# Optimization experiments

Hardware: AMD Instinct MI355X
Metric: run time of the kernel (lower is better)

## Reference

```python
import math
import jax, jax.numpy as jnp
import numpy as np

B, C, K, P, STRIDE, ITERS = 32, 32, 3, 4, 2, 3
PSIZE = P * P
EPS = 1e-6
LAMBDA = 1e-3
LN_2PI = math.log(2.0 * math.pi)


def _extract_patches(x, K, stride):
    # Replicates torch F.unfold + transpose + view exactly, including the
    # layout reinterpretation: unfold's channel dim is ordered (c, kh, kw)
    # (c slowest) but the torch code views it as (K*K, c).
    b, h, w, c = x.shape
    pad = K // 2
    oh = (h + 2 * pad - K) // stride + 1
    ow = (w + 2 * pad - K) // stride + 1
    xp = jnp.pad(x, ((0, 0), (pad, pad), (pad, pad), (0, 0)))
    sl = []
    for kh in range(K):
        for kw in range(K):
            sl.append(xp[:, kh:kh + stride * (oh - 1) + 1:stride,
                            kw:kw + stride * (ow - 1) + 1:stride, :])
    p = jnp.stack(sl, axis=-1)                 # (b, oh, ow, c, K*K)  -> (c, kh, kw) order
    p = p.reshape(b, oh, ow, c * K * K)        # flat, c slowest (matches torch unfold memory)
    patches = p.reshape(b, oh, ow, K * K, c)   # reinterpret as (K*K, c), as the torch view does
    return patches, oh, ow


def _em_routing(v, a_in, beta_u, beta_a):
    # v: (b, Bin, C, psize), a_in: (b, Bin, 1)
    b, Bin, Cc, psize = v.shape
    r = jnp.full((b, Bin, Cc, 1), 1.0 / Cc, dtype=v.dtype)
    a4 = a_in[:, :, None, :]                   # (b, Bin, 1, 1)
    a_out = None
    mu = None
    for t in range(ITERS):
        # ---- M step ----
        rr = r * a4
        rr = rr / (jnp.sum(rr, axis=2, keepdims=True) + EPS)
        r_sum = jnp.sum(rr, axis=1, keepdims=True)            # (b,1,C,1)
        coeff = rr / (r_sum + EPS)
        mu = jnp.sum(coeff * v, axis=1, keepdims=True)        # (b,1,C,psize)
        sigma_sq = jnp.sum(coeff * (v - mu) ** 2, axis=1, keepdims=True) + EPS
        sigma_sq = jnp.maximum(sigma_sq, 1e-4)
        r_sum_flat = r_sum.reshape(b, Cc, 1)
        sig_flat = jnp.maximum(sigma_sq.reshape(b, Cc, psize), 1e-4)
        cost_h = (beta_u.reshape(1, Cc, 1) + jnp.log(jnp.sqrt(sig_flat))) * r_sum_flat
        a_out = jax.nn.sigmoid(LAMBDA * (beta_a.reshape(1, Cc) - jnp.sum(cost_h, axis=2)))
        a_out = jnp.clip(a_out, 1e-4, 1.0 - 1e-4)
        mu = jnp.nan_to_num(mu, nan=0.0, posinf=1e4, neginf=-1e4)
        sigma_sq = jnp.nan_to_num(sigma_sq, nan=1e-4, posinf=1e4, neginf=1e-4)
        a_out = jnp.nan_to_num(a_out, nan=0.5, posinf=1.0 - 1e-4, neginf=1e-4)
        # ---- E step ----
        if t < ITERS - 1:
            ss = jnp.maximum(sigma_sq, 1e-4)
            ao = jnp.clip(a_out, 1e-4, 1.0 - 1e-4)
            ln_p = -(v - mu) ** 2 / (2.0 * ss) - jnp.log(jnp.sqrt(ss)) - 0.5 * LN_2PI
            ln_ap = jnp.sum(ln_p, axis=3) + jnp.log(ao.reshape(b, 1, Cc) + EPS)
            ln_ap = jnp.nan_to_num(ln_ap, nan=0.0, posinf=50.0, neginf=-50.0)
            r = jax.nn.softmax(ln_ap, axis=2)[..., None]
            r = jnp.nan_to_num(r, nan=1.0 / Cc, posinf=1.0, neginf=0.0)
    p_out = jnp.nan_to_num(mu[:, 0], nan=0.0, posinf=1e4, neginf=-1e4)  # (b, C, psize)
    a_out = jnp.nan_to_num(a_out, nan=0.5, posinf=1.0 - 1e-4, neginf=1e-4)
    return p_out, a_out


def setup_inputs() -> dict:
    key = jax.random.key(0)
    k1, k2 = jax.random.split(key)
    x = jax.random.normal(k1, (2, 16, 16, B * (PSIZE + 1)), dtype=jnp.float32)
    weights = jax.random.normal(k2, (1, K * K * B, C, PSIZE, PSIZE), dtype=jnp.float32) * 0.02
    beta_u = jnp.zeros((C,), dtype=jnp.float32)
    beta_a = jnp.zeros((C,), dtype=jnp.float32)
    return {"x": x, "weights": weights, "beta_u": beta_u, "beta_a": beta_a}


def reference(x, weights, beta_u, beta_a):
    b, h, w, c = x.shape
    patches, oh, ow = _extract_patches(x, K, STRIDE)          # (b,oh,ow,K*K,c)
    p_in = patches[..., :B * PSIZE].reshape(b * oh * ow, K * K * B, PSIZE)
    a_in = patches[..., B * PSIZE:].reshape(b * oh * ow, K * K * B, 1)
    w0 = weights[0]                                           # (K*K*B, C, psize, psize)
    v = jnp.einsum('bip,icpq->bicq', p_in, w0)                # (b*, K*K*B, C, psize)
    p_out, a_out = _em_routing(v, a_in, beta_u, beta_a)
    p_out = p_out.reshape(b, oh, ow, C * PSIZE)
    a_out = a_out.reshape(b, oh, ow, C)
    out = jnp.concatenate([p_out, a_out], axis=3)
    return p_out, a_out, out
```

## Files before the change

kernel.cpp:

```cpp
#include <hip/hip_runtime.h>
#include <hip/hip_bf16.h>
#include <math.h>

#define EPSV 1e-6f
#define LAMBDAV 1e-3f
#define LN_2PI 1.8378770664093453f

__device__ __forceinline__ float bflo(unsigned int u) {
    union { unsigned int i; float f; } x; x.i = u << 16; return x.f;
}
__device__ __forceinline__ float bfhi(unsigned int u) {
    union { unsigned int i; float f; } x; x.i = u & 0xffff0000u; return x.f;
}
__device__ __forceinline__ unsigned short f2bf(float f) {
    __hip_bfloat16 h = __float2bfloat16(f);
    return *(unsigned short*)&h;
}

typedef __attribute__((ext_vector_type(8))) short s8v;
typedef __attribute__((ext_vector_type(4))) float f4v;
typedef __attribute__((ext_vector_type(2))) int i2v;

template<int CTRL>
__device__ __forceinline__ float dpp_mv(float x) {
    return __int_as_float(__builtin_amdgcn_update_dpp(
        0, __float_as_int(x), CTRL, 0xF, 0xF, true));
}
__device__ __forceinline__ float x16_sum(float x) {
#if __has_builtin(__builtin_amdgcn_permlane16_swap)
    i2v r = __builtin_amdgcn_permlane16_swap(__float_as_int(x), __float_as_int(x), false, false);
    return __int_as_float(r.x) + __int_as_float(r.y);
#else
    return x + __int_as_float(__builtin_amdgcn_ds_swizzle(__float_as_int(x), 0x401F));
#endif
}
__device__ __forceinline__ float x16_max(float x) {
#if __has_builtin(__builtin_amdgcn_permlane16_swap)
    i2v r = __builtin_amdgcn_permlane16_swap(__float_as_int(x), __float_as_int(x), false, false);
    return fmaxf(__int_as_float(r.x), __int_as_float(r.y));
#else
    return fmaxf(x, __int_as_float(__builtin_amdgcn_ds_swizzle(__float_as_int(x), 0x401F)));
#endif
}
__device__ __forceinline__ float xhalf_sum(float x) {
#if __has_builtin(__builtin_amdgcn_permlane32_swap)
    i2v r = __builtin_amdgcn_permlane32_swap(__float_as_int(x), __float_as_int(x), false, false);
    return __int_as_float(r.x) + __int_as_float(r.y);
#else
    return x + __shfl_xor(x, 32, 64);
#endif
}
__device__ __forceinline__ float red_max32(float x) {
    x = fmaxf(x, dpp_mv<0xB1>(x));
    x = fmaxf(x, dpp_mv<0x4E>(x));
    x = fmaxf(x, dpp_mv<0x124>(x));
    x = fmaxf(x, dpp_mv<0x128>(x));
    return x16_max(x);
}
__device__ __forceinline__ float red_sum32(float x) {
    x += dpp_mv<0xB1>(x);
    x += dpp_mv<0x4E>(x);
    x += dpp_mv<0x124>(x);
    x += dpp_mv<0x128>(x);
    return x16_sum(x);
}
__device__ __forceinline__ float red_sum16(float x) {
    x += dpp_mv<0xB1>(x);
    x += dpp_mv<0x4E>(x);
    x += dpp_mv<0x124>(x);
    x += dpp_mv<0x128>(x);
    return x;
}

__global__ __launch_bounds__(256)
void conv_v_kernel(const float* __restrict__ x, const float* __restrict__ w,
                   __hip_bfloat16* __restrict__ vout)
{
    __shared__ unsigned short wb[256 * 40];
    __shared__ unsigned short pb[128 * 40];
    __shared__ unsigned short st[16 * 264];

    const int bid = blockIdx.x;
    const int i2  = bid >> 1;
    const int mh  = bid & 1;
    const int tid = threadIdx.x;

    for (int u = tid; u < 256 * 8; u += 256) {
        int r = u >> 3, j = u & 7;
        *(unsigned int*)&wb[r * 40 + 16 + j * 2] = 0;
    }
    for (int u = tid; u < 128 * 8; u += 256) {
        int r = u >> 3, j = u & 7;
        *(unsigned int*)&pb[r * 40 + 16 + j * 2] = 0;
    }
    #pragma unroll 4
    for (int u = 0; u < 16; ++u) {
        int idx = u * 256 + tid;
        int cl = idx >> 8, p = (idx >> 4) & 15, q = idx & 15;
        wb[(cl * 16 + q) * 40 + p] = f2bf(w[(size_t)i2 * 8192 + mh * 4096 + idx]);
    }
    #pragma unroll
    for (int u = 0; u < 8; ++u) {
        int idx = u * 256 + tid;
        int nn = idx >> 4, p = idx & 15;
        int e  = i2 * 16 + p;
        int k2 = e >> 9, c2 = e & 511;
        int f  = k2 * 544 + c2;
        int ci = f / 9, kk = f - ci * 9;
        int bi = nn >> 6, oi = (nn >> 3) & 7, oj = nn & 7;
        int row = 2 * oi + kk / 3 - 1;
        int col = 2 * oj + (kk - (kk / 3) * 3) - 1;
        float val = 0.f;
        if ((unsigned)row < 16u && (unsigned)col < 16u)
            val = x[((bi * 16 + row) * 16 + col) * 544 + ci];
        pb[nn * 40 + p] = f2bf(val);
    }
    __syncthreads();

    const int lane = tid & 63;
    const int wv   = tid >> 6;
    const int l16  = lane & 15;
    const int quad = lane >> 4;
    const int cq0l = wv * 64;

    s8v afrag[4], bfrag[8];
    #pragma unroll
    for (int mt = 0; mt < 4; ++mt)
        afrag[mt] = *(const s8v*)&wb[(cq0l + mt * 16 + l16) * 40 + quad * 8];
    #pragma unroll
    for (int nt = 0; nt < 8; ++nt)
        bfrag[nt] = *(const s8v*)&pb[(nt * 16 + l16) * 40 + quad * 8];

    const int srow = tid >> 4;
    const int schk = tid & 15;
    #pragma unroll
    for (int nt = 0; nt < 8; ++nt) {
        #pragma unroll
        for (int mt = 0; mt < 4; ++mt) {
            f4v acc = {0.f, 0.f, 0.f, 0.f};
            acc = __builtin_amdgcn_mfma_f32_16x16x32_bf16(afrag[mt], bfrag[nt], acc, 0, 0, 0);
            int ccol = cq0l + mt * 16 + quad * 4;
            unsigned int lo = f2bf(acc[0]) | ((unsigned int)f2bf(acc[1]) << 16);
            unsigned int hi = f2bf(acc[2]) | ((unsigned int)f2bf(acc[3]) << 16);
            uint2 pk; pk.x = lo; pk.y = hi;
            *(uint2*)&st[l16 * 264 + ccol] = pk;
        }
        __syncthreads();
        {
            uint4 d0 = *(const uint4*)&st[srow * 264 + schk * 16];
            uint4 d1 = *(const uint4*)&st[srow * 264 + schk * 16 + 8];
            int nl = nt * 16 + srow;
            unsigned short* dst = (unsigned short*)vout
                + ((size_t)nl * 288 + i2) * 512 + mh * 256 + schk * 16;
            *(uint4*)dst = d0;
            *(uint4*)(dst + 8) = d1;
        }
        __syncthreads();
    }
}

__global__ __launch_bounds__(512)
void em_sweep_kernel(const float* __restrict__ x,
                     const unsigned short* __restrict__ v,
                     const float* __restrict__ beta_u,
                     const float* __restrict__ beta_a,
                     float* __restrict__ gpart,
                     const int t)
{
    __shared__ float fct_s[288];
    __shared__ float red_s[8 * 64 * 17];
    __shared__ float mu_s[32 * 17];
    __shared__ float i2ss_s[32 * 17];
    __shared__ float kc_s[32];

    const int bid = blockIdx.x;
    const int n   = bid & 127;
    const int h   = bid >> 7;
    const int tid = threadIdx.x;
    const int bi = n >> 6, oi = (n >> 3) & 7, oj = n & 7;

    if (tid < 288) {
        int k2 = tid >> 5;
        int c2 = 512 + (tid & 31);
        int f  = k2 * 544 + c2;
        int ci = f / 9;
        int kk = f - ci * 9;
        int row = 2 * oi + kk / 3 - 1;
        int col = 2 * oj + (kk - (kk / 3) * 3) - 1;
        float a = 0.f;
        if ((unsigned)row < 16u && (unsigned)col < 16u)
            a = x[((bi * 16 + row) * 16 + col) * 544 + ci];
        fct_s[tid] = a / (a + EPSV);
    }

    if (t > 0) {
        const int c2 = tid >> 4, q2 = tid & 15;
        const float* pa = gpart + ((size_t)(t - 1) * 128 + n) * 6 * 1088;
        float S1 = 0.f, S2 = 0.f, S0 = 0.f;
        #pragma unroll
        for (int j = 0; j < 6; ++j) {
            S1 += pa[j * 1088 + tid];
            S2 += pa[j * 1088 + 512 + tid];
            S0 += pa[j * 1088 + 1024 + c2];
        }
        float invr = 1.0f / (S0 + EPSV);
        float w0  = S0 * invr;
        float m   = S1 * invr;
        float s2p = S2 * invr;
        float sig = s2p - m * m * (2.0f - w0);
        sig = fmaxf(sig + EPSV, 1e-4f);
        float hl = 0.5f * logf(sig);
        mu_s[c2 * 17 + q2]   = m;
        i2ss_s[c2 * 17 + q2] = 1.0f / (2.0f * sig);
        float shl = red_sum16(hl);
        if (q2 == 0) {
            float bu  = beta_u[c2];
            float cs  = (16.0f * bu + shl) * S0;
            float arg = LAMBDAV * (beta_a[c2] - cs);
            float ao  = 1.0f / (1.0f + expf(-arg));
            ao = fminf(fmaxf(ao, 1e-4f), 1.0f - 1e-4f);
            kc_s[c2]  = logf(ao + EPSV) - shl - 8.0f * LN_2PI;
        }
    }
    __syncthreads();

    const unsigned short* vb = v + (size_t)n * 288 * 512;
    const int wv   = tid >> 6;
    const int lane = tid & 63;
    const int c    = lane & 31;
    const int qh   = lane >> 5;
    const int qb   = qh * 8;
    const unsigned short* base = vb + c * 16 + qb;

    float mu8[8], is8[8], kcv = 0.f;
    if (t > 0) {
        #pragma unroll
        for (int j = 0; j < 8; ++j) {
            mu8[j] = mu_s[c * 17 + qb + j];
            is8[j] = i2ss_s[c * 17 + qb + j];
        }
        kcv = kc_s[c];
    }

    float s0 = 0.f, s1[8], s2[8];
    #pragma unroll
    for (int j = 0; j < 8; ++j) { s1[j] = 0.f; s2[j] = 0.f; }

    const int kofs = h * 48;

    uint4 ua = *(const uint4*)(base + (size_t)(kofs + 0 + wv) * 512);
    uint4 ub = *(const uint4*)(base + (size_t)(kofs + 8 + wv) * 512);

    #pragma unroll
    for (int kp = 0; kp < 3; ++kp) {
        const int ia = kofs + kp * 16 + wv;
        const int ib = ia + 8;
        uint4 una = ua, unb = ub;
        if (kp < 2) {
            una = *(const uint4*)(base + (size_t)(ia + 16) * 512);
            unb = *(const uint4*)(base + (size_t)(ia + 24) * 512);
        }
        float va[8], vvb[8];
        va[0] = bflo(ua.x); va[1] = bfhi(ua.x);
        va[2] = bflo(ua.y); va[3] = bfhi(ua.y);
        va[4] = bflo(ua.z); va[5] = bfhi(ua.z);
        va[6] = bflo(ua.w); va[7] = bfhi(ua.w);
        vvb[0] = bflo(ub.x); vvb[1] = bfhi(ub.x);
        vvb[2] = bflo(ub.y); vvb[3] = bfhi(ub.y);
        vvb[4] = bflo(ub.z); vvb[5] = bfhi(ub.z);
        vvb[6] = bflo(ub.w); vvb[7] = bfhi(ub.w);

        float rra, rrb;
        if (t == 0) {
            rra = fct_s[ia] * 0.03125f;
            rrb = fct_s[ib] * 0.03125f;
        } else {
            float pa = 0.f, pb2 = 0.f;
            #pragma unroll
            for (int j = 0; j < 8; ++j) {
                float da = va[j] - mu8[j];
                float db = vvb[j] - mu8[j];
                pa  += da * da * is8[j];
                pb2 += db * db * is8[j];
            }
            pa  = xhalf_sum(pa);
            pb2 = xhalf_sum(pb2);
            float acca = kcv - pa;
            float accb = kcv - pb2;
            float mxa = red_max32(acca);
            float mxb = red_max32(accb);
            float ea = __expf(acca - mxa);
            float eb = __expf(accb - mxb);
            float sa = red_sum32(ea);
            float sb = red_sum32(eb);
            rra = (ea / sa) * fct_s[ia];
            rrb = (eb / sb) * fct_s[ib];
        }

        s0 += rra + rrb;
        #pragma unroll
        for (int j = 0; j < 8; ++j) {
            s1[j] += rra * va[j] + rrb * vvb[j];
            s2[j] += rra * va[j] * va[j] + rrb * vvb[j] * vvb[j];
        }
        ua = una; ub = unb;
    }

    {
        float* dst = &red_s[(wv * 64 + lane) * 17];
        dst[0] = s0;
        #pragma unroll
        for (int j = 0; j < 8; ++j) { dst[1 + j] = s1[j]; dst[9 + j] = s2[j]; }
    }
    __syncthreads();

    {
        const int c2 = tid >> 4, q2 = tid & 15;
        const int qh2 = q2 >> 3, j2 = q2 & 7;
        float S0 = 0.f, S1 = 0.f, S2 = 0.f;
        #pragma unroll
        for (int wvi = 0; wvi < 8; ++wvi) {
            S0 += red_s[(wvi * 64 + c2) * 17];
            const float* sp = &red_s[(wvi * 64 + qh2 * 32 + c2) * 17];
            S1 += sp[1 + j2];
            S2 += sp[9 + j2];
        }
        float* po = gpart + (((size_t)t * 128 + n) * 6 + h) * 1088;
        po[tid] = S1;
        po[512 + tid] = S2;
        if (q2 == 0) po[1024 + c2] = S0;
    }
}

__global__ __launch_bounds__(512)
void em_final_kernel(const float* __restrict__ gpart,
                     const float* __restrict__ beta_u,
                     const float* __restrict__ beta_a,
                     float* __restrict__ out)
{
    __shared__ float aout_s[32];
    const int n   = blockIdx.x;
    const int tid = threadIdx.x;
    const int c2 = tid >> 4, q2 = tid & 15;

    const float* pa = gpart + ((size_t)2 * 128 + n) * 6 * 1088;
    float S1 = 0.f, S2 = 0.f, S0 = 0.f;
    #pragma unroll
    for (int j = 0; j < 6; ++j) {
        S1 += pa[j * 1088 + tid];
        S2 += pa[j * 1088 + 512 + tid];
        S0 += pa[j * 1088 + 1024 + c2];
    }
    float invr = 1.0f / (S0 + EPSV);
    float w0  = S0 * invr;
    float m   = S1 * invr;
    float s2p = S2 * invr;
    float sig = s2p - m * m * (2.0f - w0);
    sig = fmaxf(sig + EPSV, 1e-4f);
    float hl = 0.5f * logf(sig);
    float shl = red_sum16(hl);
    if (q2 == 0) {
        float bu  = beta_u[c2];
        float cs  = (16.0f * bu + shl) * S0;
        float arg = LAMBDAV * (beta_a[c2] - cs);
        float ao  = 1.0f / (1.0f + expf(-arg));
        ao = fminf(fmaxf(ao, 1e-4f), 1.0f - 1e-4f);
        if (isnan(ao)) ao = 0.5f;
        aout_s[c2] = ao;
    }
    float mu = m;
    if (isnan(mu)) mu = 0.f;
    mu = fminf(fmaxf(mu, -10000.f), 10000.f);
    out[(size_t)n * 512 + tid] = mu;
    out[69632 + (size_t)n * 544 + tid] = mu;
    __syncthreads();
    if (tid < 32) {
        float ao = aout_s[tid];
        out[65536 + n * 32 + tid] = ao;
        out[69632 + n * 544 + 512 + tid] = ao;
    }
}

extern "C" void kernel_launch(void* const* d_in, const int* in_sizes, int n_in,
                              void* d_out, int out_size, void* d_ws, size_t ws_size,
                              hipStream_t stream) {
    const float* x  = (const float*)d_in[0];
    const float* w  = (const float*)d_in[1];
    const float* bu = (const float*)d_in[2];
    const float* ba = (const float*)d_in[3];
    float* out = (float*)d_out;
    __hip_bfloat16* v = (__hip_bfloat16*)d_ws;
    float* gpart = (float*)((char*)d_ws + (40u << 20));

    conv_v_kernel<<<dim3(576), dim3(256), 0, stream>>>(x, w, v);
    em_sweep_kernel<<<dim3(768), dim3(512), 0, stream>>>(
        x, (const unsigned short*)v, bu, ba, gpart, 0);
    em_sweep_kernel<<<dim3(768), dim3(512), 0, stream>>>(
        x, (const unsigned short*)v, bu, ba, gpart, 1);
    em_sweep_kernel<<<dim3(768), dim3(512), 0, stream>>>(
        x, (const unsigned short*)v, bu, ba, gpart, 2);
    em_final_kernel<<<dim3(128), dim3(512), 0, stream>>>(gpart, bu, ba, out);
}
```

Before: 112.1 us.

## Fuse final EM step into last sweep via last-block atomic counter

```diff
diff --git a/kernel.cpp b/kernel.cpp
--- a/kernel.cpp
+++ b/kernel.cpp
@@ -71,10 +71,13 @@
     x += dpp_mv<0x128>(x);
     return x;
 }
+__device__ __forceinline__ float g_agent_load(const float* p) {
+    return __hip_atomic_load(p, __ATOMIC_RELAXED, __HIP_MEMORY_SCOPE_AGENT);
+}
 
 __global__ __launch_bounds__(256)
 void conv_v_kernel(const float* __restrict__ x, const float* __restrict__ w,
-                   __hip_bfloat16* __restrict__ vout)
+                   __hip_bfloat16* __restrict__ vout, unsigned int* __restrict__ cnt)
 {
     __shared__ unsigned short wb[256 * 40];
     __shared__ unsigned short pb[128 * 40];
@@ -85,6 +88,8 @@
     const int mh  = bid & 1;
     const int tid = threadIdx.x;
 
+    if (bid == 0 && tid < 128) cnt[tid] = 0;
+
     for (int u = tid; u < 256 * 8; u += 256) {
         int r = u >> 3, j = u & 7;
         *(unsigned int*)&wb[r * 40 + 16 + j * 2] = 0;
@@ -93,11 +98,18 @@
         int r = u >> 3, j = u & 7;
         *(unsigned int*)&pb[r * 40 + 16 + j * 2] = 0;
     }
-    #pragma unroll 4
-    for (int u = 0; u < 16; ++u) {
-        int idx = u * 256 + tid;
-        int cl = idx >> 8, p = (idx >> 4) & 15, q = idx & 15;
-        wb[(cl * 16 + q) * 40 + p] = f2bf(w[(size_t)i2 * 8192 + mh * 4096 + idx]);
+    {
+        const float* wsrc = w + (size_t)i2 * 8192 + mh * 4096;
+        #pragma unroll
+        for (int uu = 0; uu < 4; ++uu) {
+            int idx = (uu * 256 + tid) * 4;
+            float4 f = *(const float4*)&wsrc[idx];
+            int cl = idx >> 8, p = (idx >> 4) & 15, q = idx & 15;
+            wb[(cl * 16 + q + 0) * 40 + p] = f2bf(f.x);
+            wb[(cl * 16 + q + 1) * 40 + p] = f2bf(f.y);
+            wb[(cl * 16 + q + 2) * 40 + p] = f2bf(f.z);
+            wb[(cl * 16 + q + 3) * 40 + p] = f2bf(f.w);
+        }
     }
     #pragma unroll
     for (int u = 0; u < 8; ++u) {
@@ -165,6 +177,9 @@
                      const float* __restrict__ beta_u,
                      const float* __restrict__ beta_a,
                      float* __restrict__ gpart,
+                     float* __restrict__ gfct,
+                     unsigned int* __restrict__ cnt,
+                     float* __restrict__ out,
                      const int t)
 {
     __shared__ float fct_s[288];
@@ -172,6 +187,8 @@
     __shared__ float mu_s[32 * 17];
     __shared__ float i2ss_s[32 * 17];
     __shared__ float kc_s[32];
+    __shared__ float aout_s[32];
+    __shared__ unsigned int last_s;
 
     const int bid = blockIdx.x;
     const int n   = bid & 127;
@@ -179,18 +196,24 @@
     const int tid = threadIdx.x;
     const int bi = n >> 6, oi = (n >> 3) & 7, oj = n & 7;
 
-    if (tid < 288) {
-        int k2 = tid >> 5;
-        int c2 = 512 + (tid & 31);
-        int f  = k2 * 544 + c2;
-        int ci = f / 9;
-        int kk = f - ci * 9;
-        int row = 2 * oi + kk / 3 - 1;
-        int col = 2 * oj + (kk - (kk / 3) * 3) - 1;
-        float a = 0.f;
-        if ((unsigned)row < 16u && (unsigned)col < 16u)
-            a = x[((bi * 16 + row) * 16 + col) * 544 + ci];
-        fct_s[tid] = a / (a + EPSV);
+    if (t == 0) {
+        if (tid < 288) {
+            int k2 = tid >> 5;
+            int c2 = 512 + (tid & 31);
+            int f  = k2 * 544 + c2;
+            int ci = f / 9;
+            int kk = f - ci * 9;
+            int row = 2 * oi + kk / 3 - 1;
+            int col = 2 * oj + (kk - (kk / 3) * 3) - 1;
+            float a = 0.f;
+            if ((unsigned)row < 16u && (unsigned)col < 16u)
+                a = x[((bi * 16 + row) * 16 + col) * 544 + ci];
+            float fc = a / (a + EPSV);
+            fct_s[tid] = fc;
+            if (h == 0) gfct[n * 288 + tid] = fc;
+        }
+    } else {
+        if (tid < 288) fct_s[tid] = gfct[n * 288 + tid];
     }
 
     if (t > 0) {
@@ -330,54 +353,55 @@
         po[512 + tid] = S2;
         if (q2 == 0) po[1024 + c2] = S0;
     }
-}
-
-__global__ __launch_bounds__(512)
-void em_final_kernel(const float* __restrict__ gpart,
-                     const float* __restrict__ beta_u,
-                     const float* __restrict__ beta_a,
-                     float* __restrict__ out)
-{
-    __shared__ float aout_s[32];
-    const int n   = blockIdx.x;
-    const int tid = threadIdx.x;
-    const int c2 = tid >> 4, q2 = tid & 15;
-
-    const float* pa = gpart + ((size_t)2 * 128 + n) * 6 * 1088;
-    float S1 = 0.f, S2 = 0.f, S0 = 0.f;
-    #pragma unroll
-    for (int j = 0; j < 6; ++j) {
-        S1 += pa[j * 1088 + tid];
-        S2 += pa[j * 1088 + 512 + tid];
-        S0 += pa[j * 1088 + 1024 + c2];
-    }
-    float invr = 1.0f / (S0 + EPSV);
-    float w0  = S0 * invr;
-    float m   = S1 * invr;
-    float s2p = S2 * invr;
-    float sig = s2p - m * m * (2.0f - w0);
-    sig = fmaxf(sig + EPSV, 1e-4f);
-    float hl = 0.5f * logf(sig);
-    float shl = red_sum16(hl);
-    if (q2 == 0) {
-        float bu  = beta_u[c2];
-        float cs  = (16.0f * bu + shl) * S0;
-        float arg = LAMBDAV * (beta_a[c2] - cs);
-        float ao  = 1.0f / (1.0f + expf(-arg));
-        ao = fminf(fmaxf(ao, 1e-4f), 1.0f - 1e-4f);
-        if (isnan(ao)) ao = 0.5f;
-        aout_s[c2] = ao;
-    }
-    float mu = m;
-    if (isnan(mu)) mu = 0.f;
-    mu = fminf(fmaxf(mu, -10000.f), 10000.f);
-    out[(size_t)n * 512 + tid] = mu;
-    out[69632 + (size_t)n * 544 + tid] = mu;
-    __syncthreads();
-    if (tid < 32) {
-        float ao = aout_s[tid];
-        out[65536 + n * 32 + tid] = ao;
-        out[69632 + n * 544 + 512 + tid] = ao;
+
+    if (t == 2) {
+        __threadfence();
+        __syncthreads();
+        if (tid == 0) {
+            unsigned int old = __hip_atomic_fetch_add(
+                &cnt[n], 1u, __ATOMIC_ACQ_REL, __HIP_MEMORY_SCOPE_AGENT);
+            last_s = (old == 5u) ? 1u : 0u;
+        }
+        __syncthreads();
+        if (last_s) {
+            const int c2 = tid >> 4, q2 = tid & 15;
+            const float* pa = gpart + ((size_t)2 * 128 + n) * 6 * 1088;
+            float S1 = 0.f, S2 = 0.f, S0 = 0.f;
+            #pragma unroll
+            for (int j = 0; j < 6; ++j) {
+                S1 += g_agent_load(pa + j * 1088 + tid);
+                S2 += g_agent_load(pa + j * 1088 + 512 + tid);
+                S0 += g_agent_load(pa + j * 1088 + 1024 + c2);
+            }
+            float invr = 1.0f / (S0 + EPSV);
+            float w0  = S0 * invr;
+            float m   = S1 * invr;
+            float s2p = S2 * invr;
+            float sig = s2p - m * m * (2.0f - w0);
+            sig = fmaxf(sig + EPSV, 1e-4f);
+            float hl = 0.5f * logf(sig);
+            float shl = red_sum16(hl);
+            if (q2 == 0) {
+                float bu  = beta_u[c2];
+                float cs  = (16.0f * bu + shl) * S0;
+                float arg = LAMBDAV * (beta_a[c2] - cs);
+                float ao  = 1.0f / (1.0f + expf(-arg));
+                ao = fminf(fmaxf(ao, 1e-4f), 1.0f - 1e-4f);
+                if (isnan(ao)) ao = 0.5f;
+                aout_s[c2] = ao;
+            }
+            float mu = m;
+            if (isnan(mu)) mu = 0.f;
+            mu = fminf(fmaxf(mu, -10000.f), 10000.f);
+            out[(size_t)n * 512 + tid] = mu;
+            out[69632 + (size_t)n * 544 + tid] = mu;
+            __syncthreads();
+            if (tid < 32) {
+                float ao = aout_s[tid];
+                out[65536 + n * 32 + tid] = ao;
+                out[69632 + n * 544 + 512 + tid] = ao;
+            }
+        }
     }
 }
 
@@ -389,15 +413,17 @@
     const float* bu = (const float*)d_in[2];
     const float* ba = (const float*)d_in[3];
     float* out = (float*)d_out;
-    __hip_bfloat16* v = (__hip_bfloat16*)d_ws;
-    float* gpart = (float*)((char*)d_ws + (40u << 20));
-
-    conv_v_kernel<<<dim3(576), dim3(256), 0, stream>>>(x, w, v);
+    __hip_bfloat16* v  = (__hip_bfloat16*)d_ws;
+    float* gpart       = (float*)((char*)d_ws + (40u << 20));
+    float* gfct        = (float*)((char*)d_ws + (52u << 20));
+    unsigned int* cnt  = (unsigned int*)((char*)d_ws + (53u << 20));
+    const unsigned short* vv = (const unsigned short*)v;
+
+    conv_v_kernel<<<dim3(576), dim3(256), 0, stream>>>(x, w, v, cnt);
     em_sweep_kernel<<<dim3(768), dim3(512), 0, stream>>>(
-        x, (const unsigned short*)v, bu, ba, gpart, 0);
+        x, vv, bu, ba, gpart, gfct, cnt, out, 0);
     em_sweep_kernel<<<dim3(768), dim3(512), 0, stream>>>(
-        x, (const unsigned short*)v, bu, ba, gpart, 1);
+        x, vv, bu, ba, gpart, gfct, cnt, out, 1);
     em_sweep_kernel<<<dim3(768), dim3(512), 0, stream>>>(
-        x, (const unsigned short*)v, bu, ba, gpart, 2);
-    em_final_kernel<<<dim3(128), dim3(512), 0, stream>>>(gpart, bu, ba, out);
-}
+        x, vv, bu, ba, gpart, gfct, cnt, out, 2);
+}
```

After: 246.9 us. 2.2x slower.
